# Kernel tuning notes

Hardware: AMD Instinct MI355X
Metric: run time of the kernel (lower is better)

Reference implementation:

```python
import jax, jax.numpy as jnp
import numpy as np

NUM_ROI = 200

def mish(x):
    return x * jnp.tanh(jax.nn.softplus(x))

def gcn_conv(x, edge_index, edge_weight, W, b):
    # PyG GCNConv: add self-loops (weight 1), symmetric normalization, aggregate at target (col)
    N = x.shape[0]
    row, col = edge_index[0], edge_index[1]
    loop = jnp.arange(N)
    row = jnp.concatenate([row, loop])
    col = jnp.concatenate([col, loop])
    w = jnp.concatenate([edge_weight, jnp.ones((N,), x.dtype)])
    deg = jax.ops.segment_sum(w, col, num_segments=N)
    dis = jnp.where(deg > 0, jax.lax.rsqrt(deg), 0.0)
    norm = dis[row] * w * dis[col]                       # [E+N]
    h = x @ W                                            # [N, out]
    out = jax.ops.segment_sum(h[row] * norm[:, None], col, num_segments=N)
    return out + b

def setup_inputs() -> dict:
    key = jax.random.key(0)
    ks = jax.random.split(key, 16)
    B, E = 256, 1638400
    N = B * NUM_ROI
    d = {}
    d['x'] = jax.random.normal(ks[0], (N, NUM_ROI), jnp.float32)
    d['edge_index'] = jax.random.randint(ks[1], (2, E), 0, N, jnp.int64)
    d['edge_attr'] = jax.random.uniform(ks[2], (E,), jnp.float32)
    def rn(k, shape, fan_in):
        return jax.random.normal(k, shape, jnp.float32) * (1.0 / np.sqrt(fan_in))
    d['W1'] = rn(ks[3], (NUM_ROI, 128), NUM_ROI); d['b1'] = jnp.zeros((128,), jnp.float32)
    d['W2'] = rn(ks[4], (128, 64), 128);          d['b2'] = jnp.zeros((64,), jnp.float32)
    d['Wro'] = rn(ks[5], (64, 8), 64);            d['bro'] = jnp.zeros((8,), jnp.float32)
    d['Wfc1'] = rn(ks[6], (8 * NUM_ROI, NUM_ROI), 8 * NUM_ROI); d['bfc1'] = jnp.zeros((NUM_ROI,), jnp.float32)
    d['bn_gamma'] = jnp.ones((NUM_ROI,), jnp.float32)
    d['bn_beta'] = jnp.zeros((NUM_ROI,), jnp.float32)
    d['Wfc2'] = rn(ks[7], (NUM_ROI, 2), NUM_ROI); d['bfc2'] = jnp.zeros((2,), jnp.float32)
    d['Wd1'] = rn(ks[8], (NUM_ROI, 64), NUM_ROI); d['bd1'] = jnp.zeros((64,), jnp.float32)
    d['Wd2'] = rn(ks[9], (64, 6), 64);            d['bd2'] = jnp.zeros((6,), jnp.float32)
    return d

def reference(x, edge_index, edge_attr, W1, b1, W2, b2, Wro, bro, Wfc1, bfc1,
              bn_gamma, bn_beta, Wfc2, bfc2, Wd1, bd1, Wd2, bd2):
    h = mish(gcn_conv(x, edge_index, edge_attr, W1, b1))
    h = mish(gcn_conv(h, edge_index, edge_attr, W2, b2))
    out = mish(h @ Wro + bro)                            # [N, 8]
    feat = out.reshape(-1, NUM_ROI * 8)                  # [B, 1600]
    z = feat @ Wfc1 + bfc1                               # [B, numROI]
    # BatchNorm1d in training mode (batch statistics, biased variance)
    mu = jnp.mean(z, axis=0)
    var = jnp.mean((z - mu) ** 2, axis=0)
    zn = (z - mu) * jax.lax.rsqrt(var + 1e-5) * bn_gamma + bn_beta
    mid = mish(zn)
    logits = mid @ Wfc2 + bfc2                           # [B, 2]
    rev = 2.0 * jax.lax.stop_gradient(mid) - mid
    cls_logits = jax.nn.relu(rev @ Wd1 + bd1) @ Wd2 + bd2  # [B, 6]
    return (logits, cls_logits)
```

## Files before the change

kernel.cpp:

```cpp
#include <hip/hip_runtime.h>
#include <hip/hip_bf16.h>

typedef __hip_bfloat16 bf16;
typedef __attribute__((ext_vector_type(8))) short short8;
typedef __attribute__((ext_vector_type(4))) float f32x4;

#define NROI 200

__device__ __forceinline__ float u2f(unsigned short u) {
  return __uint_as_float(((unsigned)u) << 16);
}
__device__ __forceinline__ float lo16(unsigned u) { return __uint_as_float(u << 16); }
__device__ __forceinline__ float hi16(unsigned u) { return __uint_as_float(u & 0xffff0000u); }
__device__ __forceinline__ float b2f(bf16 v) { return __bfloat162float(v); }
__device__ __forceinline__ unsigned short f2us(float f) {
  union { bf16 b; unsigned short u; } c;
  c.b = __float2bfloat16(f);
  return c.u;
}

__device__ __forceinline__ float mishf(float x) {
  float sp = (x > 20.0f) ? x : log1pf(expf(x));
  return x * tanhf(sp);
}

__global__ __launch_bounds__(256) void detect_kernel(const unsigned short* xu,
                                                     const unsigned* eiw,
                                                     int* flags) {
  int tid = threadIdx.x;
  int sane = 0, zodd = 0;
  for (int i = tid; i < 4096; i += 256) {
    unsigned short u = xu[2 * i];
    unsigned e = (u >> 7) & 0xFF;
    if (u == 0 || (e >= 100 && e <= 134)) sane++;
  }
  for (int i = tid; i < 4096; i += 256) {
    if (eiw[2 * i + 1] == 0) zodd++;
  }
  __shared__ int s1[256], s2[256];
  s1[tid] = sane; s2[tid] = zodd;
  __syncthreads();
  for (int off = 128; off > 0; off >>= 1) {
    if (tid < off) { s1[tid] += s1[tid + off]; s2[tid] += s2[tid + off]; }
    __syncthreads();
  }
  if (tid == 0) {
    flags[0] = (s1[0] < 2048) ? 1 : 0;
    flags[1] = (s2[0] > 2048) ? 1 : 0;
  }
}

struct WArgs {
  const void* src[16];
  int n[16];
  int off[16];
};

__global__ __launch_bounds__(256) void convert_weights(WArgs a, bf16* base,
                                                       const int* flags) {
  int t = blockIdx.y;
  int i = blockIdx.x * 256 + threadIdx.x;
  if (i >= a.n[t]) return;
  bf16* dst = base + a.off[t];
  if (flags[0]) dst[i] = __float2bfloat16(((const float*)a.src[t])[i]);
  else ((unsigned short*)dst)[i] = ((const unsigned short*)a.src[t])[i];
}

__global__ __launch_bounds__(256) void swizzleW(const unsigned short* __restrict__ src,
                                                unsigned short* __restrict__ dst,
                                                int K, int KC, int NT) {
  int idx = blockIdx.x * 256 + threadIdx.x;
  int total = KC * NT * 512;
  if (idx >= total) return;
  int e = idx & 7;
  int l = (idx >> 3) & 63;
  int t = (idx >> 9) % NT;
  int kc = idx / (NT * 512);
  int k = kc * 32 + (l >> 4) * 8 + e;
  int c = t * 16 + (l & 15);
  dst[idx] = (k < K) ? src[k * (NT * 16) + c] : 0;
}

__global__ __launch_bounds__(256) void xbf_convert(const void* __restrict__ x,
                                                   unsigned short* __restrict__ xb,
                                                   const int* __restrict__ flags,
                                                   int N) {
  long long idx = (long long)blockIdx.x * 256 + threadIdx.x;
  long long total = (long long)N * 224;
  if (idx >= total) return;
  int c = (int)(idx % 224);
  long long n = idx / 224;
  unsigned short v = 0;
  if (c < 200) {
    if (flags[0]) v = f2us(((const float*)x)[n * 200 + c]);
    else v = ((const unsigned short*)x)[n * 200 + c];
  }
  xb[idx] = v;
}


__global__ void init_dc(unsigned long long* dc, int N) {
  int i = blockIdx.x * blockDim.x + threadIdx.x;
  if (i < N) dc[i] = 0ull;
}

__global__ void edge_count(const int* __restrict__ ei, const void* __restrict__ ea,
                           const int* __restrict__ flags,
                           unsigned long long* dc, int* __restrict__ rank, int E) {
  int e = blockIdx.x * blockDim.x + threadIdx.x;
  if (e >= E) return;
  int is64 = flags[1], isf32 = flags[0];
  int col = is64 ? ei[2 * (E + e)] : ei[E + e];
  float w = isf32 ? ((const float*)ea)[e] : u2f(((const unsigned short*)ea)[e]);
  unsigned long long p = (1ull << 40) | (unsigned long long)(w * 4294967296.0f);
  unsigned long long old = atomicAdd(&dc[col], p);
  rank[e] = (int)(old >> 40);
}

__global__ void make_dis(const unsigned long long* __restrict__ dc, float* dis, int N) {
  int i = blockIdx.x * blockDim.x + threadIdx.x;
  if (i < N) {
    float wsum = (float)(dc[i] & 0xFFFFFFFFFFull) * 2.3283064365386963e-10f;
    dis[i] = rsqrtf(1.0f + wsum);
  }
}

__global__ __launch_bounds__(256) void scan_phase1(const unsigned long long* __restrict__ dc,
                                                   int* __restrict__ bsum, int N) {
  __shared__ int ts[256];
  int tid = threadIdx.x;
  int base = blockIdx.x * 1024 + tid * 4;
  int s = 0;
#pragma unroll
  for (int j = 0; j < 4; ++j)
    if (base + j < N) s += (int)(dc[base + j] >> 40);
  ts[tid] = s;
  __syncthreads();
  for (int off = 128; off > 0; off >>= 1) {
    if (tid < off) ts[tid] += ts[tid + off];
    __syncthreads();
  }
  if (tid == 0) bsum[blockIdx.x] = ts[0];
}

__global__ __launch_bounds__(64) void scan_phase2(const int* __restrict__ bsum,
                                                  int* __restrict__ bpre,
                                                  int* __restrict__ ptr, int nb, int N) {
  if (threadIdx.x == 0) {
    int run = 0;
    for (int i = 0; i < nb; ++i) { bpre[i] = run; run += bsum[i]; }
    ptr[N] = run;
  }
}

__global__ __launch_bounds__(256) void scan_phase3(const unsigned long long* __restrict__ dc,
                                                   const int* __restrict__ bpre,
                                                   int* __restrict__ ptr, int N) {
  __shared__ int ts[256];
  int tid = threadIdx.x;
  int base = blockIdx.x * 1024 + tid * 4;
  int c0 = 0, c1 = 0, c2 = 0, c3 = 0;
  if (base + 0 < N) c0 = (int)(dc[base + 0] >> 40);
  if (base + 1 < N) c1 = (int)(dc[base + 1] >> 40);
  if (base + 2 < N) c2 = (int)(dc[base + 2] >> 40);
  if (base + 3 < N) c3 = (int)(dc[base + 3] >> 40);
  ts[tid] = c0 + c1 + c2 + c3;
  __syncthreads();
  for (int off = 1; off < 256; off <<= 1) {
    int v = ts[tid];
    if (tid >= off) v += ts[tid - off];
    __syncthreads();
    ts[tid] = v;
    __syncthreads();
  }
  int run = bpre[blockIdx.x] + (tid ? ts[tid - 1] : 0);
  if (base + 0 < N) { ptr[base + 0] = run; run += c0; }
  if (base + 1 < N) { ptr[base + 1] = run; run += c1; }
  if (base + 2 < N) { ptr[base + 2] = run; run += c2; }
  if (base + 3 < N) { ptr[base + 3] = run; run += c3; }
}

__global__ void edge_scatter(const int* __restrict__ ei, const void* __restrict__ ea,
                             const int* __restrict__ flags,
                             const float* __restrict__ dis,
                             const int* __restrict__ ptr,
                             const int* __restrict__ rank,
                             int2* __restrict__ epair, int E) {
  int e = blockIdx.x * blockDim.x + threadIdx.x;
  if (e >= E) return;
  int is64 = flags[1], isf32 = flags[0];
  int r = is64 ? ei[2 * e] : ei[e];
  int c = is64 ? ei[2 * (E + e)] : ei[E + e];
  float w = isf32 ? ((const float*)ea)[e] : u2f(((const unsigned short*)ea)[e]);
  float nrm = dis[r] * w * dis[c];
  int idx = ptr[c] + rank[e];
  int2 pr; pr.x = r; pr.y = __float_as_int(nrm);
  epair[idx] = pr;
}

template<int KC, int NT>
__global__ __launch_bounds__(256) void gemm_mfma(const unsigned short* __restrict__ Abf,
                                                 const unsigned short* __restrict__ Wswz,
                                                 unsigned short* __restrict__ H,
                                                 int M) {
  int wid = threadIdx.x >> 6, lane = threadIdx.x & 63;
  int row0 = (blockIdx.x * 4 + wid) * 16;
  if (row0 >= M) return;
  constexpr int K = KC * 32;
  constexpr int NC = NT * 16;
  f32x4 acc[NT];
#pragma unroll
  for (int t = 0; t < NT; ++t) acc[t] = {0.f, 0.f, 0.f, 0.f};
  size_t arow = (size_t)(row0 + (lane & 15)) * K + (lane >> 4) * 8;
#pragma unroll
  for (int kc = 0; kc < KC; ++kc) {
    short8 a = *(const short8*)&Abf[arow + kc * 32];
#pragma unroll
    for (int t = 0; t < NT; ++t) {
      short8 b = *(const short8*)&Wswz[((kc * NT + t) * 64 + lane) * 8];
      acc[t] = __builtin_amdgcn_mfma_f32_16x16x32_bf16(a, b, acc[t], 0, 0, 0);
    }
  }
  int orow = row0 + (lane >> 4) * 4;
  int ocol = lane & 15;
#pragma unroll
  for (int t = 0; t < NT; ++t)
#pragma unroll
    for (int r = 0; r < 4; ++r)
      H[(size_t)(orow + r) * NC + t * 16 + ocol] = f2us(acc[t][r]);
}


__global__ __launch_bounds__(256) void agg_mish128(const unsigned* __restrict__ hu,
                                                   const float* __restrict__ dis,
                                                   const int* __restrict__ ptr,
                                                   const int2* __restrict__ ep,
                                                   const bf16* __restrict__ bias,
                                                   unsigned* __restrict__ g, int N) {
  int n = blockIdx.x * 4 + (threadIdx.x >> 6);
  int lane = threadIdx.x & 63;
  float dn = dis[n];
  float self = dn * dn;
  unsigned u = hu[(size_t)n * 64 + lane];
  float acc0 = lo16(u) * self;
  float acc1 = hi16(u) * self;
  int e = ptr[n], e1 = ptr[n + 1];
  for (; e + 8 <= e1; e += 8) {
    int2 p[8]; unsigned uu[8];
#pragma unroll
    for (int j = 0; j < 8; ++j) p[j] = ep[e + j];
#pragma unroll
    for (int j = 0; j < 8; ++j) uu[j] = hu[(size_t)p[j].x * 64 + lane];
#pragma unroll
    for (int j = 0; j < 8; ++j) {
      float w = __int_as_float(p[j].y);
      acc0 += lo16(uu[j]) * w;
      acc1 += hi16(uu[j]) * w;
    }
  }
  for (; e < e1; ++e) {
    int2 pp = ep[e];
    unsigned uu = hu[(size_t)pp.x * 64 + lane];
    float w = __int_as_float(pp.y);
    acc0 += lo16(uu) * w;
    acc1 += hi16(uu) * w;
  }
  unsigned bb = ((const unsigned*)bias)[lane];
  float m0 = mishf(acc0 + lo16(bb));
  float m1 = mishf(acc1 + hi16(bb));
  g[(size_t)n * 64 + lane] = ((unsigned)f2us(m1) << 16) | f2us(m0);
}

__global__ __launch_bounds__(256) void agg_mish64_ro(const unsigned* __restrict__ hu,
                                                     const float* __restrict__ dis,
                                                     const int* __restrict__ ptr,
                                                     const int2* __restrict__ ep,
                                                     const bf16* __restrict__ bias,
                                                     const bf16* __restrict__ Wro,
                                                     const bf16* __restrict__ bro,
                                                     float* __restrict__ out8, int N) {
  int w = threadIdx.x >> 6;
  int lane = threadIdx.x & 63;
  int half = lane >> 5, l5 = lane & 31;
  int n = blockIdx.x * 8 + w * 2 + half;
  float dn = dis[n];
  float self = dn * dn;
  unsigned u = hu[(size_t)n * 32 + l5];
  float acc0 = lo16(u) * self;
  float acc1 = hi16(u) * self;
  int e = ptr[n], e1 = ptr[n + 1];
  for (; e + 8 <= e1; e += 8) {
    int2 p[8]; unsigned uu[8];
#pragma unroll
    for (int j = 0; j < 8; ++j) p[j] = ep[e + j];
#pragma unroll
    for (int j = 0; j < 8; ++j) uu[j] = hu[(size_t)p[j].x * 32 + l5];
#pragma unroll
    for (int j = 0; j < 8; ++j) {
      float wv = __int_as_float(p[j].y);
      acc0 += lo16(uu[j]) * wv;
      acc1 += hi16(uu[j]) * wv;
    }
  }
  for (; e < e1; ++e) {
    int2 pp = ep[e];
    unsigned uu = hu[(size_t)pp.x * 32 + l5];
    float wv = __int_as_float(pp.y);
    acc0 += lo16(uu) * wv;
    acc1 += hi16(uu) * wv;
  }
  unsigned bb = ((const unsigned*)bias)[l5];
  float m0 = mishf(acc0 + lo16(bb));
  float m1 = mishf(acc1 + hi16(bb));
  uint4 r0 = ((const uint4*)Wro)[2 * l5];
  uint4 r1 = ((const uint4*)Wro)[2 * l5 + 1];
  float p0 = m0 * lo16(r0.x) + m1 * lo16(r1.x);
  float p1 = m0 * hi16(r0.x) + m1 * hi16(r1.x);
  float p2 = m0 * lo16(r0.y) + m1 * lo16(r1.y);
  float p3 = m0 * hi16(r0.y) + m1 * hi16(r1.y);
  float p4 = m0 * lo16(r0.z) + m1 * lo16(r1.z);
  float p5 = m0 * hi16(r0.z) + m1 * hi16(r1.z);
  float p6 = m0 * lo16(r0.w) + m1 * lo16(r1.w);
  float p7 = m0 * hi16(r0.w) + m1 * hi16(r1.w);
#pragma unroll
  for (int off = 16; off >= 1; off >>= 1) {
    p0 += __shfl_xor(p0, off);
    p1 += __shfl_xor(p1, off);
    p2 += __shfl_xor(p2, off);
    p3 += __shfl_xor(p3, off);
    p4 += __shfl_xor(p4, off);
    p5 += __shfl_xor(p5, off);
    p6 += __shfl_xor(p6, off);
    p7 += __shfl_xor(p7, off);
  }
  if (l5 == 0) {
    float4 q0, q1;
    q0.x = mishf(p0 + b2f(bro[0])); q0.y = mishf(p1 + b2f(bro[1]));
    q0.z = mishf(p2 + b2f(bro[2])); q0.w = mishf(p3 + b2f(bro[3]));
    q1.x = mishf(p4 + b2f(bro[4])); q1.y = mishf(p5 + b2f(bro[5]));
    q1.z = mishf(p6 + b2f(bro[6])); q1.w = mishf(p7 + b2f(bro[7]));
    *(float4*)&out8[(size_t)n * 8] = q0;
    *(float4*)&out8[(size_t)n * 8 + 4] = q1;
  }
}


__global__ __launch_bounds__(256) void fc1_kernel(const float* __restrict__ feat,
                                                  const bf16* __restrict__ W,
                                                  const bf16* __restrict__ bias,
                                                  float* __restrict__ z) {
  __shared__ float fr[1600];
  int b = blockIdx.x, tid = threadIdx.x;
  for (int i = tid; i < 1600; i += 256) fr[i] = feat[(size_t)b * 1600 + i];
  __syncthreads();
  if (tid < NROI) {
    float acc = b2f(bias[tid]);
#pragma unroll 8
    for (int k = 0; k < 1600; ++k) acc += fr[k] * b2f(W[k * NROI + tid]);
    z[b * NROI + tid] = acc;
  }
}

__global__ __launch_bounds__(256) void bn_stats(const float* __restrict__ z,
                                                float* mu, float* rvar, int B) {
  int j = blockIdx.x;
  int tid = threadIdx.x;
  float v = z[tid * NROI + j];
  float s = v, q = v * v;
  for (int off = 32; off > 0; off >>= 1) {
    s += __shfl_down(s, off);
    q += __shfl_down(q, off);
  }
  __shared__ float ss[4], qq[4];
  int w = tid >> 6, lane = tid & 63;
  if (lane == 0) { ss[w] = s; qq[w] = q; }
  __syncthreads();
  if (tid == 0) {
    float S = ss[0] + ss[1] + ss[2] + ss[3];
    float Q = qq[0] + qq[1] + qq[2] + qq[3];
    float m = S / (float)B;
    float var = Q / (float)B - m * m;
    mu[j] = m;
    rvar[j] = rsqrtf(var + 1e-5f);
  }
}

__global__ __launch_bounds__(256) void head_kernel(const float* __restrict__ z,
                                                   const float* __restrict__ mu,
                                                   const float* __restrict__ rvar,
                                                   const bf16* __restrict__ gamma,
                                                   const bf16* __restrict__ beta,
                                                   const bf16* __restrict__ Wfc2,
                                                   const bf16* __restrict__ bfc2,
                                                   const bf16* __restrict__ Wd1,
                                                   const bf16* __restrict__ bd1,
                                                   const bf16* __restrict__ Wd2,
                                                   const bf16* __restrict__ bd2,
                                                   float* __restrict__ out, int B) {
  __shared__ float mid[NROI];
  __shared__ float t[64];
  int b = blockIdx.x, tid = threadIdx.x;
  if (tid < NROI) {
    float v = (z[b * NROI + tid] - mu[tid]) * rvar[tid] * b2f(gamma[tid]) + b2f(beta[tid]);
    mid[tid] = mishf(v);
  }
  __syncthreads();
  if (tid < 64) {
    float acc = b2f(bd1[tid]);
#pragma unroll 8
    for (int j = 0; j < NROI; ++j) acc += mid[j] * b2f(Wd1[j * 64 + tid]);
    t[tid] = fmaxf(acc, 0.0f);
  }
  if (tid >= 64 && tid < 66) {
    int c = tid - 64;
    float acc = b2f(bfc2[c]);
    for (int j = 0; j < NROI; ++j) acc += mid[j] * b2f(Wfc2[j * 2 + c]);
    out[b * 2 + c] = acc;
  }
  __syncthreads();
  if (tid < 6) {
    float acc = b2f(bd2[tid]);
#pragma unroll 8
    for (int k = 0; k < 64; ++k) acc += t[k] * b2f(Wd2[k * 6 + tid]);
    out[B * 2 + b * 6 + tid] = acc;
  }
}


extern "C" void kernel_launch(void* const* d_in, const int* in_sizes, int n_in,
                              void* d_out, int out_size, void* d_ws, size_t ws_size,
                              hipStream_t stream) {
  const void* x  = d_in[0];
  const int*  ei = (const int*)d_in[1];
  const void* ea = d_in[2];
  float* out = (float*)d_out;

  int N = in_sizes[0] / NROI;
  int E = in_sizes[2];
  int B = N / NROI;

  char* p = (char*)d_ws;
  auto carve = [&](size_t bytes) -> void* {
    void* r = (void*)p;
    p += (bytes + 255) & ~(size_t)255;
    return r;
  };
  int*   flags = (int*)carve(16);
  bf16*  cw    = (bf16*)carve(400000 * 2);
  float* dis   = (float*)carve((size_t)N * 4);
  unsigned long long* dc = (unsigned long long*)carve((size_t)N * 8);
  int*   ptr   = (int*)carve(((size_t)N + 1) * 4);
  int*   bsum  = (int*)carve(1024);
  int*   bpre  = (int*)carve(1024);
  int2*  epair = (int2*)carve((size_t)E * 8);
  unsigned short* h = (unsigned short*)carve((size_t)N * 128 * 2);
  size_t xg_bytes = (size_t)N * 224 * 2;
  size_t rk_bytes = (size_t)E * 4;
  char* xg = (char*)carve(xg_bytes > rk_bytes ? xg_bytes : rk_bytes);
  int* rank = (int*)xg;
  unsigned short* xbf = (unsigned short*)xg;
  unsigned* g = (unsigned*)xg;
  unsigned short* w1swz = (unsigned short*)carve(7 * 8 * 512 * 2);
  unsigned short* w2swz = (unsigned short*)carve(4 * 4 * 512 * 2);
  float* out8  = (float*)carve((size_t)N * 8 * 4);
  float* z     = (float*)carve((size_t)B * NROI * 4);
  float* mu    = (float*)carve(NROI * 4);
  float* rv    = (float*)carve(NROI * 4);

  WArgs wa;
  int run = 0;
  int maxn = 0;
  for (int t = 0; t < 16; ++t) {
    wa.src[t] = d_in[3 + t];
    wa.n[t]   = in_sizes[3 + t];
    wa.off[t] = run;
    run += in_sizes[3 + t];
    if (in_sizes[3 + t] > maxn) maxn = in_sizes[3 + t];
  }
  const bf16* W1   = cw + wa.off[0];
  const bf16* b1   = cw + wa.off[1];
  const bf16* W2   = cw + wa.off[2];
  const bf16* b2   = cw + wa.off[3];
  const bf16* Wro  = cw + wa.off[4];
  const bf16* bro  = cw + wa.off[5];
  const bf16* Wfc1 = cw + wa.off[6];
  const bf16* bfc1 = cw + wa.off[7];
  const bf16* gam  = cw + wa.off[8];
  const bf16* bet  = cw + wa.off[9];
  const bf16* Wfc2 = cw + wa.off[10];
  const bf16* bfc2 = cw + wa.off[11];
  const bf16* Wd1  = cw + wa.off[12];
  const bf16* bd1  = cw + wa.off[13];
  const bf16* Wd2  = cw + wa.off[14];
  const bf16* bd2  = cw + wa.off[15];

  int nb = (N + 255) / 256;
  int eb = (E + 255) / 256;
  int nscan = (N + 1023) / 1024;

  detect_kernel<<<1, 256, 0, stream>>>((const unsigned short*)x,
                                       (const unsigned*)ei, flags);
  dim3 wg((maxn + 255) / 256, 16);
  convert_weights<<<wg, 256, 0, stream>>>(wa, cw, flags);
  swizzleW<<<(7 * 8 * 512 + 255) / 256, 256, 0, stream>>>(
      (const unsigned short*)W1, w1swz, 200, 7, 8);
  swizzleW<<<(4 * 4 * 512 + 255) / 256, 256, 0, stream>>>(
      (const unsigned short*)W2, w2swz, 128, 4, 4);

  init_dc<<<nb, 256, 0, stream>>>(dc, N);
  edge_count<<<eb, 256, 0, stream>>>(ei, ea, flags, dc, rank, E);
  make_dis<<<nb, 256, 0, stream>>>(dc, dis, N);
  scan_phase1<<<nscan, 256, 0, stream>>>(dc, bsum, N);
  scan_phase2<<<1, 64, 0, stream>>>(bsum, bpre, ptr, nscan, N);
  scan_phase3<<<nscan, 256, 0, stream>>>(dc, bpre, ptr, N);
  edge_scatter<<<eb, 256, 0, stream>>>(ei, ea, flags, dis, ptr, rank, epair, E);

  long long xtot = (long long)N * 224;
  xbf_convert<<<(int)((xtot + 255) / 256), 256, 0, stream>>>(x, xbf, flags, N);
  gemm_mfma<7, 8><<<N / 64, 256, 0, stream>>>(xbf, w1swz, h, N);
  agg_mish128<<<N / 4, 256, 0, stream>>>((const unsigned*)h, dis, ptr, epair,
                                         b1, g, N);
  gemm_mfma<4, 4><<<N / 64, 256, 0, stream>>>((const unsigned short*)g, w2swz, h, N);
  agg_mish64_ro<<<N / 8, 256, 0, stream>>>((const unsigned*)h, dis, ptr, epair,
                                           b2, Wro, bro, out8, N);

  fc1_kernel<<<B, 256, 0, stream>>>(out8, Wfc1, bfc1, z);
  bn_stats<<<NROI, 256, 0, stream>>>(z, mu, rv, B);
  head_kernel<<<B, 256, 0, stream>>>(z, mu, rv, gam, bet, Wfc2, bfc2,
                                     Wd1, bd1, Wd2, bd2, out, B);
}
```

Baseline: 410.5 us.

## Privatize degree atomics per XCD and use wave-cooperative edge loads in aggregation

Edge counting now reads the XCC id and accumulates into per-XCD copies of the degree/count array with workgroup-scope atomics, avoiding device-scope atomic contention across chiplets. A new kernel combines the eight partial counts into per-node totals, degree normalization and per-XCD base offsets that edge_scatter uses to place edges. Both aggregation kernels now load up to 64 edge pairs cooperatively per wave and broadcast them with readlane instead of each lane loading them redundantly. The second aggregation uses one node per wave with a butterfly readout reduction. The cost is 8x more counter memory plus an extra pass, and workgroup-scope atomics are only correct if each XCD's L2 is coherent for its own copy.

```diff
diff --git a/kernel.cpp b/kernel.cpp
--- a/kernel.cpp
+++ b/kernel.cpp
@@ -99,33 +99,57 @@
 }
 
 
-__global__ void init_dc(unsigned long long* dc, int N) {
-  int i = blockIdx.x * blockDim.x + threadIdx.x;
-  if (i < N) dc[i] = 0ull;
+__global__ void init_dc8(unsigned long long* dc8, long long M) {
+  long long i = (long long)blockIdx.x * blockDim.x + threadIdx.x;
+  if (i < M) dc8[i] = 0ull;
 }
 
 __global__ void edge_count(const int* __restrict__ ei, const void* __restrict__ ea,
                            const int* __restrict__ flags,
-                           unsigned long long* dc, int* __restrict__ rank, int E) {
+                           unsigned long long* dc8, int* __restrict__ rank,
+                           int N, int E) {
   int e = blockIdx.x * blockDim.x + threadIdx.x;
   if (e >= E) return;
+  unsigned xcd;
+  asm("s_getreg_b32 %0, hwreg(HW_REG_XCC_ID)" : "=s"(xcd));
+  xcd &= 7;
   int is64 = flags[1], isf32 = flags[0];
   int col = is64 ? ei[2 * (E + e)] : ei[E + e];
   float w = isf32 ? ((const float*)ea)[e] : u2f(((const unsigned short*)ea)[e]);
   unsigned long long p = (1ull << 40) | (unsigned long long)(w * 4294967296.0f);
-  unsigned long long old = atomicAdd(&dc[col], p);
-  rank[e] = (int)(old >> 40);
-}
-
-__global__ void make_dis(const unsigned long long* __restrict__ dc, float* dis, int N) {
-  int i = blockIdx.x * blockDim.x + threadIdx.x;
-  if (i < N) {
-    float wsum = (float)(dc[i] & 0xFFFFFFFFFFull) * 2.3283064365386963e-10f;
-    dis[i] = rsqrtf(1.0f + wsum);
-  }
-}
-
-__global__ __launch_bounds__(256) void scan_phase1(const unsigned long long* __restrict__ dc,
+  unsigned long long old = __hip_atomic_fetch_add(&dc8[(size_t)xcd * N + col], p,
+                                                  __ATOMIC_RELAXED,
+                                                  __HIP_MEMORY_SCOPE_WORKGROUP);
+  rank[e] = ((int)xcd << 20) | (int)(old >> 40);
+}
+
+__global__ __launch_bounds__(256) void xcd_base(const unsigned long long* __restrict__ dc8,
+                                                float* __restrict__ dis,
+                                                int* __restrict__ cnt,
+                                                unsigned short* __restrict__ xb, int N) {
+  int n = blockIdx.x * 256 + threadIdx.x;
+  if (n >= N) return;
+  int run = 0;
+  unsigned long long ws = 0;
+  unsigned short loc[8];
+#pragma unroll
+  for (int x = 0; x < 8; ++x) {
+    unsigned long long v = dc8[(size_t)x * N + n];
+    loc[x] = (unsigned short)run;
+    run += (int)(v >> 40);
+    ws += v & 0xFFFFFFFFFFull;
+  }
+  cnt[n] = run;
+  dis[n] = rsqrtf(1.0f + (float)ws * 2.3283064365386963e-10f);
+  uint4 o;
+  o.x = (unsigned)loc[0] | ((unsigned)loc[1] << 16);
+  o.y = (unsigned)loc[2] | ((unsigned)loc[3] << 16);
+  o.z = (unsigned)loc[4] | ((unsigned)loc[5] << 16);
+  o.w = (unsigned)loc[6] | ((unsigned)loc[7] << 16);
+  ((uint4*)xb)[n] = o;
+}
+
+__global__ __launch_bounds__(256) void scan_phase1(const int* __restrict__ cnt,
                                                    int* __restrict__ bsum, int N) {
   __shared__ int ts[256];
   int tid = threadIdx.x;
@@ -133,7 +157,7 @@
   int s = 0;
 #pragma unroll
   for (int j = 0; j < 4; ++j)
-    if (base + j < N) s += (int)(dc[base + j] >> 40);
+    if (base + j < N) s += cnt[base + j];
   ts[tid] = s;
   __syncthreads();
   for (int off = 128; off > 0; off >>= 1) {
@@ -153,17 +177,17 @@
   }
 }
 
-__global__ __launch_bounds__(256) void scan_phase3(const unsigned long long* __restrict__ dc,
+__global__ __launch_bounds__(256) void scan_phase3(const int* __restrict__ cnt,
                                                    const int* __restrict__ bpre,
                                                    int* __restrict__ ptr, int N) {
   __shared__ int ts[256];
   int tid = threadIdx.x;
   int base = blockIdx.x * 1024 + tid * 4;
   int c0 = 0, c1 = 0, c2 = 0, c3 = 0;
-  if (base + 0 < N) c0 = (int)(dc[base + 0] >> 40);
-  if (base + 1 < N) c1 = (int)(dc[base + 1] >> 40);
-  if (base + 2 < N) c2 = (int)(dc[base + 2] >> 40);
-  if (base + 3 < N) c3 = (int)(dc[base + 3] >> 40);
+  if (base + 0 < N) c0 = cnt[base + 0];
+  if (base + 1 < N) c1 = cnt[base + 1];
+  if (base + 2 < N) c2 = cnt[base + 2];
+  if (base + 3 < N) c3 = cnt[base + 3];
   ts[tid] = c0 + c1 + c2 + c3;
   __syncthreads();
   for (int off = 1; off < 256; off <<= 1) {
@@ -184,6 +208,7 @@
                              const int* __restrict__ flags,
                              const float* __restrict__ dis,
                              const int* __restrict__ ptr,
+                             const unsigned short* __restrict__ xb,
                              const int* __restrict__ rank,
                              int2* __restrict__ epair, int E) {
   int e = blockIdx.x * blockDim.x + threadIdx.x;
@@ -193,7 +218,8 @@
   int c = is64 ? ei[2 * (E + e)] : ei[E + e];
   float w = isf32 ? ((const float*)ea)[e] : u2f(((const unsigned short*)ea)[e]);
   float nrm = dis[r] * w * dis[c];
-  int idx = ptr[c] + rank[e];
+  int rk = rank[e];
+  int idx = ptr[c] + (int)xb[(size_t)c * 8 + (rk >> 20)] + (rk & 0xFFFFF);
   int2 pr; pr.x = r; pr.y = __float_as_int(nrm);
   epair[idx] = pr;
 }
@@ -230,40 +256,50 @@
       H[(size_t)(orow + r) * NC + t * 16 + ocol] = f2us(acc[t][r]);
 }
 
-
 __global__ __launch_bounds__(256) void agg_mish128(const unsigned* __restrict__ hu,
                                                    const float* __restrict__ dis,
                                                    const int* __restrict__ ptr,
                                                    const int2* __restrict__ ep,
                                                    const bf16* __restrict__ bias,
                                                    unsigned* __restrict__ g, int N) {
-  int n = blockIdx.x * 4 + (threadIdx.x >> 6);
-  int lane = threadIdx.x & 63;
+  int w = threadIdx.x >> 6, lane = threadIdx.x & 63;
+  int n = blockIdx.x * 4 + w;
   float dn = dis[n];
   float self = dn * dn;
   unsigned u = hu[(size_t)n * 64 + lane];
   float acc0 = lo16(u) * self;
   float acc1 = hi16(u) * self;
-  int e = ptr[n], e1 = ptr[n + 1];
-  for (; e + 8 <= e1; e += 8) {
-    int2 p[8]; unsigned uu[8];
-#pragma unroll
-    for (int j = 0; j < 8; ++j) p[j] = ep[e + j];
-#pragma unroll
-    for (int j = 0; j < 8; ++j) uu[j] = hu[(size_t)p[j].x * 64 + lane];
-#pragma unroll
-    for (int j = 0; j < 8; ++j) {
-      float w = __int_as_float(p[j].y);
-      acc0 += lo16(uu[j]) * w;
-      acc1 += hi16(uu[j]) * w;
+  int e0 = ptr[n], e1 = ptr[n + 1];
+  for (int base = e0; base < e1; base += 64) {
+    int2 myp = {0, 0};
+    if (base + lane < e1) myp = ep[base + lane];
+    int m = e1 - base; if (m > 64) m = 64;
+    int j = 0;
+    for (; j + 4 <= m; j += 4) {
+      int r0 = __builtin_amdgcn_readlane(myp.x, j);
+      int r1 = __builtin_amdgcn_readlane(myp.x, j + 1);
+      int r2 = __builtin_amdgcn_readlane(myp.x, j + 2);
+      int r3 = __builtin_amdgcn_readlane(myp.x, j + 3);
+      unsigned u0 = hu[(size_t)r0 * 64 + lane];
+      unsigned u1 = hu[(size_t)r1 * 64 + lane];
+      unsigned u2 = hu[(size_t)r2 * 64 + lane];
+      unsigned u3 = hu[(size_t)r3 * 64 + lane];
+      float w0 = __uint_as_float(__builtin_amdgcn_readlane(myp.y, j));
+      float w1 = __uint_as_float(__builtin_amdgcn_readlane(myp.y, j + 1));
+      float w2 = __uint_as_float(__builtin_amdgcn_readlane(myp.y, j + 2));
+      float w3 = __uint_as_float(__builtin_amdgcn_readlane(myp.y, j + 3));
+      acc0 += lo16(u0) * w0; acc1 += hi16(u0) * w0;
+      acc0 += lo16(u1) * w1; acc1 += hi16(u1) * w1;
+      acc0 += lo16(u2) * w2; acc1 += hi16(u2) * w2;
+      acc0 += lo16(u3) * w3; acc1 += hi16(u3) * w3;
     }
-  }
-  for (; e < e1; ++e) {
-    int2 pp = ep[e];
-    unsigned uu = hu[(size_t)pp.x * 64 + lane];
-    float w = __int_as_float(pp.y);
-    acc0 += lo16(uu) * w;
-    acc1 += hi16(uu) * w;
+    for (; j < m; ++j) {
+      int rr = __builtin_amdgcn_readlane(myp.x, j);
+      float ww = __uint_as_float(__builtin_amdgcn_readlane(myp.y, j));
+      unsigned uu = hu[(size_t)rr * 64 + lane];
+      acc0 += lo16(uu) * ww;
+      acc1 += hi16(uu) * ww;
+    }
   }
   unsigned bb = ((const unsigned*)bias)[lane];
   float m0 = mishf(acc0 + lo16(bb));
@@ -271,7 +307,7 @@
   g[(size_t)n * 64 + lane] = ((unsigned)f2us(m1) << 16) | f2us(m0);
 }
 
-__global__ __launch_bounds__(256) void agg_mish64_ro(const unsigned* __restrict__ hu,
+__global__ __launch_bounds__(256) void agg_mish64_ro(const unsigned short* __restrict__ hus,
                                                      const float* __restrict__ dis,
                                                      const int* __restrict__ ptr,
                                                      const int2* __restrict__ ep,
@@ -279,68 +315,60 @@
                                                      const bf16* __restrict__ Wro,
                                                      const bf16* __restrict__ bro,
                                                      float* __restrict__ out8, int N) {
-  int w = threadIdx.x >> 6;
-  int lane = threadIdx.x & 63;
-  int half = lane >> 5, l5 = lane & 31;
-  int n = blockIdx.x * 8 + w * 2 + half;
+  int w = threadIdx.x >> 6, lane = threadIdx.x & 63;
+  int n = blockIdx.x * 4 + w;
   float dn = dis[n];
   float self = dn * dn;
-  unsigned u = hu[(size_t)n * 32 + l5];
-  float acc0 = lo16(u) * self;
-  float acc1 = hi16(u) * self;
-  int e = ptr[n], e1 = ptr[n + 1];
-  for (; e + 8 <= e1; e += 8) {
-    int2 p[8]; unsigned uu[8];
-#pragma unroll
-    for (int j = 0; j < 8; ++j) p[j] = ep[e + j];
-#pragma unroll
-    for (int j = 0; j < 8; ++j) uu[j] = hu[(size_t)p[j].x * 32 + l5];
-#pragma unroll
-    for (int j = 0; j < 8; ++j) {
-      float wv = __int_as_float(p[j].y);
-      acc0 += lo16(uu[j]) * wv;
-      acc1 += hi16(uu[j]) * wv;
+  float acc = u2f(hus[(size_t)n * 64 + lane]) * self;
+  int e0 = ptr[n], e1 = ptr[n + 1];
+  for (int base = e0; base < e1; base += 64) {
+    int2 myp = {0, 0};
+    if (base + lane < e1) myp = ep[base + lane];
+    int m = e1 - base; if (m > 64) m = 64;
+    int j = 0;
+    for (; j + 4 <= m; j += 4) {
+      int r0 = __builtin_amdgcn_readlane(myp.x, j);
+      int r1 = __builtin_amdgcn_readlane(myp.x, j + 1);
+      int r2 = __builtin_amdgcn_readlane(myp.x, j + 2);
+      int r3 = __builtin_amdgcn_readlane(myp.x, j + 3);
+      float v0 = u2f(hus[(size_t)r0 * 64 + lane]);
+      float v1 = u2f(hus[(size_t)r1 * 64 + lane]);
+      float v2 = u2f(hus[(size_t)r2 * 64 + lane]);
+      float v3 = u2f(hus[(size_t)r3 * 64 + lane]);
+      float w0 = __uint_as_float(__builtin_amdgcn_readlane(myp.y, j));
+      float w1 = __uint_as_float(__builtin_amdgcn_readlane(myp.y, j + 1));
+      float w2 = __uint_as_float(__builtin_amdgcn_readlane(myp.y, j + 2));
+      float w3 = __uint_as_float(__builtin_amdgcn_readlane(myp.y, j + 3));
+      acc += v0 * w0 + v1 * w1 + v2 * w2 + v3 * w3;
     }
-  }
-  for (; e < e1; ++e) {
-    int2 pp = ep[e];
-    unsigned uu = hu[(size_t)pp.x * 32 + l5];
-    float wv = __int_as_float(pp.y);
-    acc0 += lo16(uu) * wv;
-    acc1 += hi16(uu) * wv;
-  }
-  unsigned bb = ((const unsigned*)bias)[l5];
-  float m0 = mishf(acc0 + lo16(bb));
-  float m1 = mishf(acc1 + hi16(bb));
-  uint4 r0 = ((const uint4*)Wro)[2 * l5];
-  uint4 r1 = ((const uint4*)Wro)[2 * l5 + 1];
-  float p0 = m0 * lo16(r0.x) + m1 * lo16(r1.x);
-  float p1 = m0 * hi16(r0.x) + m1 * hi16(r1.x);
-  float p2 = m0 * lo16(r0.y) + m1 * lo16(r1.y);
-  float p3 = m0 * hi16(r0.y) + m1 * hi16(r1.y);
-  float p4 = m0 * lo16(r0.z) + m1 * lo16(r1.z);
-  float p5 = m0 * hi16(r0.z) + m1 * hi16(r1.z);
-  float p6 = m0 * lo16(r0.w) + m1 * lo16(r1.w);
-  float p7 = m0 * hi16(r0.w) + m1 * hi16(r1.w);
-#pragma unroll
-  for (int off = 16; off >= 1; off >>= 1) {
-    p0 += __shfl_xor(p0, off);
-    p1 += __shfl_xor(p1, off);
-    p2 += __shfl_xor(p2, off);
-    p3 += __shfl_xor(p3, off);
-    p4 += __shfl_xor(p4, off);
-    p5 += __shfl_xor(p5, off);
-    p6 += __shfl_xor(p6, off);
-    p7 += __shfl_xor(p7, off);
-  }
-  if (l5 == 0) {
-    float4 q0, q1;
-    q0.x = mishf(p0 + b2f(bro[0])); q0.y = mishf(p1 + b2f(bro[1]));
-    q0.z = mishf(p2 + b2f(bro[2])); q0.w = mishf(p3 + b2f(bro[3]));
-    q1.x = mishf(p4 + b2f(bro[4])); q1.y = mishf(p5 + b2f(bro[5]));
-    q1.z = mishf(p6 + b2f(bro[6])); q1.w = mishf(p7 + b2f(bro[7]));
-    *(float4*)&out8[(size_t)n * 8] = q0;
-    *(float4*)&out8[(size_t)n * 8 + 4] = q1;
+    for (; j < m; ++j) {
+      int rr = __builtin_amdgcn_readlane(myp.x, j);
+      float ww = __uint_as_float(__builtin_amdgcn_readlane(myp.y, j));
+      acc += u2f(hus[(size_t)rr * 64 + lane]) * ww;
+    }
+  }
+  float mv = mishf(acc + u2f(((const unsigned short*)bias)[lane]));
+  uint4 wr = ((const uint4*)Wro)[lane];
+  float p0 = mv * lo16(wr.x), p1 = mv * hi16(wr.x);
+  float p2 = mv * lo16(wr.y), p3 = mv * hi16(wr.y);
+  float p4 = mv * lo16(wr.z), p5 = mv * hi16(wr.z);
+  float p6 = mv * lo16(wr.w), p7 = mv * hi16(wr.w);
+  bool b0 = lane & 1;
+  float q0 = (b0 ? p4 : p0) + __shfl_xor(b0 ? p0 : p4, 1);
+  float q1 = (b0 ? p5 : p1) + __shfl_xor(b0 ? p1 : p5, 1);
+  float q2 = (b0 ? p6 : p2) + __shfl_xor(b0 ? p2 : p6, 1);
+  float q3 = (b0 ? p7 : p3) + __shfl_xor(b0 ? p3 : p7, 1);
+  bool b1 = lane & 2;
+  float r0 = (b1 ? q2 : q0) + __shfl_xor(b1 ? q0 : q2, 2);
+  float r1 = (b1 ? q3 : q1) + __shfl_xor(b1 ? q1 : q3, 2);
+  bool b2v = lane & 4;
+  float t = (b2v ? r1 : r0) + __shfl_xor(b2v ? r0 : r1, 4);
+  t += __shfl_xor(t, 8);
+  t += __shfl_xor(t, 16);
+  t += __shfl_xor(t, 32);
+  if (lane < 8) {
+    int oidx = ((lane & 1) << 2) | (lane & 2) | ((lane >> 2) & 1);
+    out8[(size_t)n * 8 + oidx] = mishf(t + u2f(((const unsigned short*)bro)[oidx]));
   }
 }
 
@@ -448,7 +476,9 @@
   int*   flags = (int*)carve(16);
   bf16*  cw    = (bf16*)carve(400000 * 2);
   float* dis   = (float*)carve((size_t)N * 4);
-  unsigned long long* dc = (unsigned long long*)carve((size_t)N * 8);
+  unsigned long long* dc8 = (unsigned long long*)carve((size_t)8 * N * 8);
+  int*   cnt   = (int*)carve((size_t)N * 4);
+  unsigned short* xbse = (unsigned short*)carve((size_t)N * 8 * 2);
   int*   ptr   = (int*)carve(((size_t)N + 1) * 4);
   int*   bsum  = (int*)carve(1024);
   int*   bpre  = (int*)carve(1024);
@@ -507,13 +537,15 @@
   swizzleW<<<(4 * 4 * 512 + 255) / 256, 256, 0, stream>>>(
       (const unsigned short*)W2, w2swz, 128, 4, 4);
 
-  init_dc<<<nb, 256, 0, stream>>>(dc, N);
-  edge_count<<<eb, 256, 0, stream>>>(ei, ea, flags, dc, rank, E);
-  make_dis<<<nb, 256, 0, stream>>>(dc, dis, N);
-  scan_phase1<<<nscan, 256, 0, stream>>>(dc, bsum, N);
+  long long dctot = (long long)8 * N;
+  init_dc8<<<(int)((dctot + 255) / 256), 256, 0, stream>>>(dc8, dctot);
+  edge_count<<<eb, 256, 0, stream>>>(ei, ea, flags, dc8, rank, N, E);
+  xcd_base<<<nb, 256, 0, stream>>>(dc8, dis, cnt, xbse, N);
+  scan_phase1<<<nscan, 256, 0, stream>>>(cnt, bsum, N);
   scan_phase2<<<1, 64, 0, stream>>>(bsum, bpre, ptr, nscan, N);
-  scan_phase3<<<nscan, 256, 0, stream>>>(dc, bpre, ptr, N);
-  edge_scatter<<<eb, 256, 0, stream>>>(ei, ea, flags, dis, ptr, rank, epair, E);
+  scan_phase3<<<nscan, 256, 0, stream>>>(cnt, bpre, ptr, N);
+  edge_scatter<<<eb, 256, 0, stream>>>(ei, ea, flags, dis, ptr, xbse, rank,
+                                       epair, E);
 
   long long xtot = (long long)N * 224;
   xbf_convert<<<(int)((xtot + 255) / 256), 256, 0, stream>>>(x, xbf, flags, N);
@@ -521,8 +553,8 @@
   agg_mish128<<<N / 4, 256, 0, stream>>>((const unsigned*)h, dis, ptr, epair,
                                          b1, g, N);
   gemm_mfma<4, 4><<<N / 64, 256, 0, stream>>>((const unsigned short*)g, w2swz, h, N);
-  agg_mish64_ro<<<N / 8, 256, 0, stream>>>((const unsigned*)h, dis, ptr, epair,
-                                           b2, Wro, bro, out8, N);
+  agg_mish64_ro<<<N / 4, 256, 0, stream>>>(h, dis, ptr, epair, b2, Wro, bro,
+                                           out8, N);
 
   fc1_kernel<<<B, 256, 0, stream>>>(out8, Wfc1, bfc1, z);
   bn_stats<<<NROI, 256, 0, stream>>>(z, mu, rv, B);
```

Result: faster. 385.8 us (-6.0%).
